# Optimization experiments

Hardware: AMD Instinct MI355X
Metric: run time of the kernel (lower is better)

Reference implementation:

```python
import jax, jax.numpy as jnp
import numpy as np

SEQ_LEN = 256
VOCAB = 50000
EMBED = 300
PROJ = 200
ATT = 200
CLS = 3
B = 128


def setup_inputs() -> dict:
    key = jax.random.key(0)
    ks = jax.random.split(key, 16)
    s = lambda d: 1.0 / np.sqrt(d)
    return {
        "x1": jax.random.randint(ks[0], (B, SEQ_LEN), 0, VOCAB, dtype=jnp.int32),
        "x2": jax.random.randint(ks[1], (B, SEQ_LEN), 0, VOCAB, dtype=jnp.int32),
        "emb": jax.random.normal(ks[2], (VOCAB, EMBED), jnp.float32),
        # intra-attention forward_product FC (shared for x1/x2 via AUTO_REUSE)
        "Wi": jax.random.normal(ks[3], (EMBED, ATT), jnp.float32) * s(EMBED),
        "bi": jnp.zeros((ATT,), jnp.float32),
        "b_dist": jax.random.normal(ks[4], (1,), jnp.float32) * 0.1,
        # embed-scope projection (input is concat[x, xp] -> 2*EMBED), linear
        "Wp": jax.random.normal(ks[5], (2 * EMBED, PROJ), jnp.float32) * s(2 * EMBED),
        "bp": jnp.zeros((PROJ,), jnp.float32),
        # attent forward_product FC (shared)
        "Wa": jax.random.normal(ks[6], (PROJ, ATT), jnp.float32) * s(PROJ),
        "ba": jnp.zeros((ATT,), jnp.float32),
        # compare FC (shared, dim = input dim = 2*PROJ)
        "Wc": jax.random.normal(ks[7], (2 * PROJ, 2 * PROJ), jnp.float32) * s(2 * PROJ),
        "bc": jnp.zeros((2 * PROJ,), jnp.float32),
        # aggregate FC -> class logits (linear)
        "Wg": jax.random.normal(ks[8], (4 * PROJ, CLS), jnp.float32) * s(4 * PROJ),
        "bg": jnp.zeros((CLS,), jnp.float32),
    }


def _seq_mask(x):
    # tf.count_nonzero + tf.sequence_mask -> [B, L, 1] float mask
    size = jnp.sum((x != 0).astype(jnp.float32), axis=1)  # [B]
    m = (jnp.arange(SEQ_LEN)[None, :] < size[:, None]).astype(jnp.float32)
    return m[:, :, None]


def _intra(x, Wi, bi, b_dist):
    # forward_product on (x, x): relu FC then bilinear product -> [B, L, L]
    f = jax.nn.relu(x @ Wi + bi)
    att = jnp.einsum("bid,bjd->bij", f, f)
    idx = jnp.arange(SEQ_LEN)
    dist = jnp.abs(idx[None, :] - idx[:, None])
    bias = b_dist[0] * (dist >= 10).astype(jnp.float32)  # [L, L]
    xp = jnp.einsum("bik,bkj->bij", jax.nn.softmax(att + bias[None], axis=2), x)
    return jnp.concatenate([x, xp], axis=2)  # [B, L, 2*EMBED]


def reference(x1, x2, emb, Wi, bi, b_dist, Wp, bp, Wa, ba, Wc, bc, Wg, bg):
    mask1, mask2 = _seq_mask(x1), _seq_mask(x2)  # [B, L, 1]

    # embedding lookup with L2-normalized table
    emb_n = emb / jnp.linalg.norm(emb, axis=1, keepdims=True)
    e1, e2 = emb_n[x1], emb_n[x2]  # [B, L, EMBED]

    # intra-attention (distance-biased self alignment), doubles feature dim
    h1 = _intra(e1, Wi, bi, b_dist)
    h2 = _intra(e2, Wi, bi, b_dist)

    # linear projection to PROJ
    p1 = h1 @ Wp + bp  # [B, L, PROJ]
    p2 = h2 @ Wp + bp

    # attent: forward_product sim + mask + dual-axis softmax alignments
    a1 = jax.nn.relu(p1 @ Wa + ba)
    a2 = jax.nn.relu(p2 @ Wa + ba)
    sim = jnp.einsum("bid,bjd->bij", a1, a2)  # [B, L, L]
    sim = sim * (mask1 * jnp.swapaxes(mask2, 1, 2))
    alpha = jnp.einsum("bki,bkj->bij", jax.nn.softmax(sim, axis=1), p1)
    beta = jnp.einsum("bik,bkj->bij", jax.nn.softmax(sim, axis=2), p2)

    # compare (shared relu FC)
    v1 = jax.nn.relu(jnp.concatenate([p1, beta], 2) @ Wc + bc)
    v2 = jax.nn.relu(jnp.concatenate([p2, alpha], 2) @ Wc + bc)

    # aggregate: masked sum pooling + linear classifier
    v1 = jnp.sum(v1 * mask1, axis=1)  # [B, 2*PROJ]
    v2 = jnp.sum(v2 * mask2, axis=1)
    return jnp.concatenate([v1, v2], 1) @ Wg + bg  # [B, CLS]
```

## Files before the change

### kernel.cpp

```cpp
#include <hip/hip_runtime.h>
#include <math.h>

#define LSEQ 256
#define NB   128

typedef unsigned short u16;
typedef unsigned int   u32;
typedef __attribute__((ext_vector_type(8))) short bf16x8;
typedef __attribute__((ext_vector_type(4))) float f32x4;

static __device__ __forceinline__ u16 f2bf(float x) {
    union { float f; u32 u; } v; v.f = x;
    const u32 r = v.u + 0x7fffu + ((v.u >> 16) & 1u);
    return (u16)(r >> 16);
}
static __device__ __forceinline__ void glds16(const u16* src, u16* dst) {
    __builtin_amdgcn_global_load_lds(
        (const __attribute__((address_space(1))) u32*)src,
        (__attribute__((address_space(3))) u32*)dst, 16, 0, 0);
}

template<int EPI, bool BIAS, bool RELU>
__global__ __launch_bounds__(512)
void gemm(const u16* __restrict__ A, int lda,
          const u16* __restrict__ B, int ldb,
          u16* __restrict__ C, int ldc,
          const float* __restrict__ bias, int Nbias,
          float* __restrict__ pool, const float* __restrict__ pmask,
          int K, int Nwrite)
{
    __shared__ u16 As[128 * 64];
    __shared__ u16 Bs[256 * 64];

    const int m0 = blockIdx.y * 128;
    const int n0 = blockIdx.x * 256;
    const int t = threadIdx.x;
    const int lane = t & 63;
    const int w = t >> 6;
    const int wm = w >> 2;
    const int wn = w & 3;
    const int lr = lane & 15;
    const int lg = lane >> 4;

    f32x4 acc[4][4] = {};

    for (int k0 = 0; k0 < K; k0 += 64) {
#pragma unroll
        for (int i = 0; i < 2; ++i) {
            const int ch = w * 2 + i;
            const int row = (ch << 3) + (lane >> 3);
            const int slot = (lane & 7) ^ (row & 7);
            glds16(A + (long long)(m0 + row) * lda + k0 + (slot << 3), &As[ch << 9]);
        }
#pragma unroll
        for (int i = 0; i < 4; ++i) {
            const int ch = w * 4 + i;
            const int row = (ch << 3) + (lane >> 3);
            const int slot = (lane & 7) ^ (row & 7);
            glds16(B + (long long)(n0 + row) * ldb + k0 + (slot << 3), &Bs[ch << 9]);
        }
        __syncthreads();
#pragma unroll
        for (int kk = 0; kk < 2; ++kk) {
            bf16x8 af[4], bf[4];
#pragma unroll
            for (int mi = 0; mi < 4; ++mi) {
                const int row = wm * 64 + mi * 16 + lr;
                const int slot = ((kk << 2) + lg) ^ (row & 7);
                af[mi] = *reinterpret_cast<const bf16x8*>(&As[row * 64 + (slot << 3)]);
            }
#pragma unroll
            for (int ni = 0; ni < 4; ++ni) {
                const int row = wn * 64 + ni * 16 + lr;
                const int slot = ((kk << 2) + lg) ^ (row & 7);
                bf[ni] = *reinterpret_cast<const bf16x8*>(&Bs[row * 64 + (slot << 3)]);
            }
#pragma unroll
            for (int mi = 0; mi < 4; ++mi)
#pragma unroll
                for (int ni = 0; ni < 4; ++ni)
                    acc[mi][ni] = __builtin_amdgcn_mfma_f32_16x16x32_bf16(
                        af[mi], bf[ni], acc[mi][ni], 0, 0, 0);
        }
        __syncthreads();
    }

    const int rbase = lg << 2;
    if (EPI == 0) {
#pragma unroll
        for (int ni = 0; ni < 4; ++ni) {
            const int gc = n0 + wn * 64 + ni * 16 + lr;
            if (gc >= Nwrite) continue;
            float bcv = 0.f;
            if (BIAS) bcv = (gc < Nbias) ? bias[gc] : 0.f;
#pragma unroll
            for (int mi = 0; mi < 4; ++mi) {
#pragma unroll
                for (int r = 0; r < 4; ++r) {
                    const long long gr = m0 + wm * 64 + mi * 16 + rbase + r;
                    float x = acc[mi][ni][r];
                    if (BIAS) x += bcv;
                    if (RELU) x = fmaxf(x, 0.f);
                    C[gr * ldc + gc] = f2bf(x);
                }
            }
        }
    } else {
        __syncthreads();
        float* pool_s = reinterpret_cast<float*>(As);
        for (int i = t; i < 256; i += 512) pool_s[i] = 0.f;
        __syncthreads();
        const int b_lin = m0 >> 8;
        const int side  = b_lin >> 7;
        const int bb    = b_lin & 127;
        const float* mk = pmask + b_lin * 256 + (m0 & 255);
        float mrow[4][4];
#pragma unroll
        for (int mi = 0; mi < 4; ++mi)
#pragma unroll
            for (int r = 0; r < 4; ++r)
                mrow[mi][r] = mk[wm * 64 + mi * 16 + rbase + r];
#pragma unroll
        for (int ni = 0; ni < 4; ++ni) {
            const int lc = wn * 64 + ni * 16 + lr;
            const int gc = n0 + lc;
            const float bcv = (BIAS && gc < Nbias) ? bias[gc] : 0.f;
            float cs = 0.f;
#pragma unroll
            for (int mi = 0; mi < 4; ++mi)
#pragma unroll
                for (int r = 0; r < 4; ++r)
                    cs += fmaxf(acc[mi][ni][r] + bcv, 0.f) * mrow[mi][r];
            cs += __shfl_xor(cs, 16, 64);
            cs += __shfl_xor(cs, 32, 64);
            if (lg == 0) atomicAdd(&pool_s[lc], cs);
        }
        __syncthreads();
        for (int i = t; i < 256; i += 512) {
            const int gc = n0 + i;
            if (gc < Nwrite) atomicAdd(&pool[bb * 800 + side * 400 + gc], pool_s[i]);
        }
    }
}

template<int MODE>
__global__ __launch_bounds__(512)
void fattn(const u16* __restrict__ QK, u16* __restrict__ Hb,
           u16* __restrict__ CMP, u16* __restrict__ CMP2,
           const float* __restrict__ M1, const float* __restrict__ M2,
           const float* __restrict__ b_dist)
{
    constexpr int NVT = (MODE == 0) ? 5 : 4;
    __shared__ char shmem[57344];
    u16* Ks = (u16*)shmem;
    u16* Qs = (u16*)(shmem + 32768);
    float* red  = (float*)(shmem + 49152);
    float* red2 = (float*)(shmem + 51200);
    u16* Pc = (u16*)shmem;
    u16* Vc = (u16*)(shmem + 16384);

    const int bz = blockIdx.x;
    int b, half, rowoff, ldv, ldc, Nwrite;
    const u16 *Kp, *Qp, *Vp;
    u16* Cp;
    const float *mrow = nullptr, *mcol = nullptr;
    if (MODE == 0) {
        b = (bz & 7) + (bz >> 4) * 8;
        half = (bz >> 3) & 1;
        Kp = QK + (long long)b * 65536;
        Qp = Kp;
        Vp = Hb + (long long)b * 163840; ldv = 640;
        Cp = Hb + (long long)b * 163840 + half * 128 * 640 + 320;
        ldc = 640; Nwrite = 320; rowoff = half * 128;
    } else {
        const int xcd = bz & 7, j = bz >> 3;
        const int sib = j & 3;
        b = xcd + (j >> 2) * 8;
        half = sib & 1;
        const int v = sib >> 1;
        const u16* a1 = QK + (long long)b * 65536;
        const u16* a2 = QK + 32768LL * 256 + (long long)b * 65536;
        u16* P1 = CMP  + (long long)b * 114688;
        u16* P2 = CMP2 + (long long)b * 114688;
        if (v == 0) { Qp = a1 + half * 128 * 256; Kp = a2; Vp = P2;
                      Cp = P1 + half * 128 * 448 + 200;
                      mrow = M1 + b * 256 + half * 128; mcol = M2 + b * 256; }
        else        { Qp = a2 + half * 128 * 256; Kp = a1; Vp = P1;
                      Cp = P2 + half * 128 * 448 + 200;
                      mrow = M2 + b * 256 + half * 128; mcol = M1 + b * 256; }
        ldv = 448; ldc = 448; Nwrite = 248; rowoff = 0;
    }

    const int t = threadIdx.x, lane = t & 63, w = t >> 6;
    const int lr = lane & 15, lg = lane >> 4;
    const int wk = w >> 1, wr = w & 1;
    const int wr2 = w >> 2, wc = w & 3;

    f32x4 acc[4][4] = {};
    for (int k0 = 0; k0 < 256; k0 += 64) {
#pragma unroll
        for (int i = 0; i < 4; ++i) {
            const int ch = w * 4 + i;
            const int row = (ch << 3) + (lane >> 3);
            const int slot = (lane & 7) ^ (row & 7);
            glds16(Kp + (long long)row * 256 + k0 + (slot << 3), &Ks[ch << 9]);
        }
        if (MODE != 0) {
#pragma unroll
            for (int i = 0; i < 2; ++i) {
                const int ch = w * 2 + i;
                const int row = (ch << 3) + (lane >> 3);
                const int slot = (lane & 7) ^ (row & 7);
                glds16(Qp + (long long)row * 256 + k0 + (slot << 3), &Qs[ch << 9]);
            }
        }
        __syncthreads();
#pragma unroll
        for (int kk = 0; kk < 2; ++kk) {
            bf16x8 kf[4], qf[4];
#pragma unroll
            for (int ki = 0; ki < 4; ++ki) {
                const int row = wk * 64 + ki * 16 + lr;
                const int slot = ((kk << 2) + lg) ^ (row & 7);
                kf[ki] = *reinterpret_cast<const bf16x8*>(&Ks[row * 64 + (slot << 3)]);
            }
#pragma unroll
            for (int qi = 0; qi < 4; ++qi) {
                if (MODE == 0) {
                    const int row = rowoff + wr * 64 + qi * 16 + lr;
                    const int slot = ((kk << 2) + lg) ^ (row & 7);
                    qf[qi] = *reinterpret_cast<const bf16x8*>(&Ks[row * 64 + (slot << 3)]);
                } else {
                    const int row = wr * 64 + qi * 16 + lr;
                    const int slot = ((kk << 2) + lg) ^ (row & 7);
                    qf[qi] = *reinterpret_cast<const bf16x8*>(&Qs[row * 64 + (slot << 3)]);
                }
            }
#pragma unroll
            for (int ki = 0; ki < 4; ++ki)
#pragma unroll
                for (int qi = 0; qi < 4; ++qi)
                    acc[ki][qi] = __builtin_amdgcn_mfma_f32_16x16x32_bf16(
                        kf[ki], qf[qi], acc[ki][qi], 0, 0, 0);
        }
        __syncthreads();
    }

    if (MODE == 1) {
        float mr[4], mc[4][4];
#pragma unroll
        for (int qi = 0; qi < 4; ++qi) mr[qi] = mrow[wr * 64 + qi * 16 + lr];
#pragma unroll
        for (int ki = 0; ki < 4; ++ki)
#pragma unroll
            for (int r = 0; r < 4; ++r)
                mc[ki][r] = mcol[wk * 64 + ki * 16 + (lg << 2) + r];
#pragma unroll
        for (int ki = 0; ki < 4; ++ki)
#pragma unroll
            for (int qi = 0; qi < 4; ++qi)
#pragma unroll
                for (int r = 0; r < 4; ++r)
                    acc[ki][qi][r] *= mr[qi] * mc[ki][r];
    } else {
        const float bd = b_dist[0];
#pragma unroll
        for (int ki = 0; ki < 4; ++ki)
#pragma unroll
            for (int qi = 0; qi < 4; ++qi)
#pragma unroll
                for (int r = 0; r < 4; ++r) {
                    const int irow = rowoff + wr * 64 + qi * 16 + lr;
                    const int jcol = wk * 64 + ki * 16 + (lg << 2) + r;
                    const int d = irow > jcol ? irow - jcol : jcol - irow;
                    if (d >= 10) acc[ki][qi][r] += bd;
                }
    }

    float mx[4];
#pragma unroll
    for (int qi = 0; qi < 4; ++qi) {
        float m_ = -1e30f;
#pragma unroll
        for (int ki = 0; ki < 4; ++ki)
#pragma unroll
            for (int r = 0; r < 4; ++r) m_ = fmaxf(m_, acc[ki][qi][r]);
        m_ = fmaxf(m_, __shfl_xor(m_, 16, 64));
        m_ = fmaxf(m_, __shfl_xor(m_, 32, 64));
        mx[qi] = m_;
    }
    if (lg == 0) {
#pragma unroll
        for (int qi = 0; qi < 4; ++qi)
            red[(wr * 64 + qi * 16 + lr) * 4 + wk] = mx[qi];
    }
    __syncthreads();
    float sm[4];
#pragma unroll
    for (int qi = 0; qi < 4; ++qi) {
        const int row = wr * 64 + qi * 16 + lr;
        const float m_ = fmaxf(fmaxf(red[row * 4 + 0], red[row * 4 + 1]),
                               fmaxf(red[row * 4 + 2], red[row * 4 + 3]));
        float s_ = 0.f;
#pragma unroll
        for (int ki = 0; ki < 4; ++ki)
#pragma unroll
            for (int r = 0; r < 4; ++r) {
                const float e_ = expf(acc[ki][qi][r] - m_);
                acc[ki][qi][r] = e_;
                s_ += e_;
            }
        s_ += __shfl_xor(s_, 16, 64);
        s_ += __shfl_xor(s_, 32, 64);
        sm[qi] = s_;
    }
    if (lg == 0) {
#pragma unroll
        for (int qi = 0; qi < 4; ++qi)
            red2[(wr * 64 + qi * 16 + lr) * 4 + wk] = sm[qi];
    }
    __syncthreads();
#pragma unroll
    for (int qi = 0; qi < 4; ++qi) {
        const int row = wr * 64 + qi * 16 + lr;
        const float rs = 1.0f / (red2[row * 4 + 0] + red2[row * 4 + 1]
                               + red2[row * 4 + 2] + red2[row * 4 + 3]);
#pragma unroll
        for (int ki = 0; ki < 4; ++ki)
#pragma unroll
            for (int r = 0; r < 4; ++r) acc[ki][qi][r] *= rs;
    }
    __syncthreads();

    f32x4 opv[4][NVT] = {};
    for (int c = 0; c < 4; ++c) {
        {
            const int n4 = (t & 63) << 2;
            const int k8 = (t >> 6) << 3;
            union { uint2 q2[8]; u16 s[32]; } uq;
#pragma unroll
            for (int i = 0; i < 8; ++i)
                uq.q2[i] = *reinterpret_cast<const uint2*>(
                    Vp + (long long)(c * 64 + k8 + i) * ldv + n4);
#pragma unroll
            for (int j = 0; j < 4; ++j) {
                const int row = n4 + j;
                const u32 v0 = (u32)uq.s[j]      | ((u32)uq.s[4 + j]  << 16);
                const u32 v1 = (u32)uq.s[8 + j]  | ((u32)uq.s[12 + j] << 16);
                const u32 v2 = (u32)uq.s[16 + j] | ((u32)uq.s[20 + j] << 16);
                const u32 v3 = (u32)uq.s[24 + j] | ((u32)uq.s[28 + j] << 16);
                const int slot = (t >> 6) ^ (row & 7);
                *reinterpret_cast<uint4*>(&Vc[row * 64 + (slot << 3)]) =
                    make_uint4(v0, v1, v2, v3);
            }
            if (NVT == 5 && t < 128) {
                const int n4b = 256 + ((t & 15) << 2);
                const int k8b = (t >> 4) << 3;
                union { uint2 q2[8]; u16 s[32]; } ub;
#pragma unroll
                for (int i = 0; i < 8; ++i)
                    ub.q2[i] = *reinterpret_cast<const uint2*>(
                        Vp + (long long)(c * 64 + k8b + i) * ldv + n4b);
#pragma unroll
                for (int j = 0; j < 4; ++j) {
                    const int row = n4b + j;
                    const u32 v0 = (u32)ub.s[j]      | ((u32)ub.s[4 + j]  << 16);
                    const u32 v1 = (u32)ub.s[8 + j]  | ((u32)ub.s[12 + j] << 16);
                    const u32 v2 = (u32)ub.s[16 + j] | ((u32)ub.s[20 + j] << 16);
                    const u32 v3 = (u32)ub.s[24 + j] | ((u32)ub.s[28 + j] << 16);
                    const int slot = (t >> 4) ^ (row & 7);
                    *reinterpret_cast<uint4*>(&Vc[row * 64 + (slot << 3)]) =
                        make_uint4(v0, v1, v2, v3);
                }
            }
        }
        if (wk == c) {
#pragma unroll
            for (int qi = 0; qi < 4; ++qi) {
                const int qrow = wr * 64 + qi * 16 + lr;
#pragma unroll
                for (int ki = 0; ki < 4; ++ki) {
                    const u32 lo = (u32)f2bf(acc[ki][qi][0]) | ((u32)f2bf(acc[ki][qi][1]) << 16);
                    const u32 hi = (u32)f2bf(acc[ki][qi][2]) | ((u32)f2bf(acc[ki][qi][3]) << 16);
                    const int slot = ((ki << 1) + (lg >> 1)) ^ (qrow & 7);
                    *reinterpret_cast<uint2*>(
                        (char*)Pc + qrow * 128 + (slot << 4) + ((lg & 1) << 3)) =
                        make_uint2(lo, hi);
                }
            }
        }
        __syncthreads();
#pragma unroll
        for (int kk = 0; kk < 2; ++kk) {
            bf16x8 pa[4], vb[NVT];
#pragma unroll
            for (int qi = 0; qi < 4; ++qi) {
                const int row = wr2 * 64 + qi * 16 + lr;
                const int slot = ((kk << 2) + lg) ^ (row & 7);
                pa[qi] = *reinterpret_cast<const bf16x8*>(&Pc[row * 64 + (slot << 3)]);
            }
#pragma unroll
            for (int vi = 0; vi < NVT; ++vi) {
                const int row = wc * (NVT * 16) + vi * 16 + lr;
                const int slot = ((kk << 2) + lg) ^ (row & 7);
                vb[vi] = *reinterpret_cast<const bf16x8*>(&Vc[row * 64 + (slot << 3)]);
            }
#pragma unroll
            for (int qi = 0; qi < 4; ++qi)
#pragma unroll
                for (int vi = 0; vi < NVT; ++vi)
                    opv[qi][vi] = __builtin_amdgcn_mfma_f32_16x16x32_bf16(
                        pa[qi], vb[vi], opv[qi][vi], 0, 0, 0);
        }
        __syncthreads();
    }

#pragma unroll
    for (int qi = 0; qi < 4; ++qi)
#pragma unroll
        for (int vi = 0; vi < NVT; ++vi) {
            const int gc = wc * (NVT * 16) + vi * 16 + lr;
            if (gc >= Nwrite) continue;
#pragma unroll
            for (int r = 0; r < 4; ++r) {
                const int qrow = wr2 * 64 + qi * 16 + (lg << 2) + r;
                Cp[(long long)qrow * ldc + gc] = f2bf(opv[qi][vi][r]);
            }
        }
}

__global__ __launch_bounds__(256)
void prep_w(const float* __restrict__ src, int srcRows, int srcCols,
            u16* __restrict__ dst, int dstCols, int dstTotal,
            int seg1, int seg2start)
{
    const int idx = blockIdx.x * 256 + threadIdx.x;
    if (idx >= dstTotal) return;
    const int n = idx / dstCols, k = idx - n * dstCols;
    int sr = -1;
    if (k < seg1) sr = k;
    else if (k >= seg2start && (k - seg2start) < (srcRows - seg1)) sr = seg1 + (k - seg2start);
    u16 v = 0;
    if (n < srcCols && sr >= 0) v = f2bf(src[(long long)sr * srcCols + n]);
    dst[idx] = v;
}

__global__ __launch_bounds__(256)
void zero_pool(float* __restrict__ p)
{
    p[blockIdx.x * 256 + threadIdx.x] = 0.f;
}

__global__ __launch_bounds__(256)
void make_mask(const int* __restrict__ x, float* __restrict__ mask)
{
    const int b = blockIdx.x;
    const int t = threadIdx.x;
    int nz = (x[b * LSEQ + t] != 0) ? 1 : 0;
#pragma unroll
    for (int o = 32; o; o >>= 1) nz += __shfl_xor(nz, o, 64);
    __shared__ int red[4];
    if ((t & 63) == 0) red[t >> 6] = nz;
    __syncthreads();
    const int size = red[0] + red[1] + red[2] + red[3];
    mask[b * LSEQ + t] = (t < size) ? 1.0f : 0.0f;
}

__global__ __launch_bounds__(256)
void gather_norm(const int* __restrict__ x, const float* __restrict__ emb,
                 u16* __restrict__ h)
{
    const int t = threadIdx.x;
    const int lane = t & 63;
    const long long row = (long long)blockIdx.x * 4 + (t >> 6);
    const int tok = x[row];
    const float* er = emb + (long long)tok * 300;
    float vals[5];
    float ss = 0.f;
#pragma unroll
    for (int i = 0; i < 5; ++i) {
        const int c = lane + i * 64;
        const float v = (c < 300) ? er[c] : 0.f;
        vals[i] = v;
        ss = fmaf(v, v, ss);
    }
#pragma unroll
    for (int o = 32; o; o >>= 1) ss += __shfl_xor(ss, o, 64);
    const float inv = 1.0f / sqrtf(ss);
    u16* out = h + row * 640;
#pragma unroll
    for (int i = 0; i < 5; ++i) {
        const int c = lane + i * 64;
        out[c] = f2bf(vals[i] * inv);
    }
}

__global__ __launch_bounds__(256)
void final_fc(const float* __restrict__ pooled, const float* __restrict__ Wg,
              const float* __restrict__ bg, float* __restrict__ out)
{
    const int b = blockIdx.x;
    const int t = threadIdx.x;
    float a0 = 0.f, a1 = 0.f, a2 = 0.f;
    for (int k = t; k < 800; k += 256) {
        const float p = pooled[(long long)b * 800 + k];
        a0 = fmaf(p, Wg[k * 3 + 0], a0);
        a1 = fmaf(p, Wg[k * 3 + 1], a1);
        a2 = fmaf(p, Wg[k * 3 + 2], a2);
    }
#pragma unroll
    for (int o = 32; o; o >>= 1) {
        a0 += __shfl_xor(a0, o, 64);
        a1 += __shfl_xor(a1, o, 64);
        a2 += __shfl_xor(a2, o, 64);
    }
    __shared__ float r0[4], r1[4], r2[4];
    if ((t & 63) == 0) { r0[t >> 6] = a0; r1[t >> 6] = a1; r2[t >> 6] = a2; }
    __syncthreads();
    if (t == 0) {
        out[b * 3 + 0] = r0[0] + r0[1] + r0[2] + r0[3] + bg[0];
        out[b * 3 + 1] = r1[0] + r1[1] + r1[2] + r1[3] + bg[1];
        out[b * 3 + 2] = r2[0] + r2[1] + r2[2] + r2[3] + bg[2];
    }
}

extern "C" void kernel_launch(void* const* d_in, const int* in_sizes, int n_in,
                              void* d_out, int out_size, void* d_ws, size_t ws_size,
                              hipStream_t stream)
{
    (void)in_sizes; (void)n_in; (void)out_size; (void)ws_size;

    const int*   x1     = (const int*)  d_in[0];
    const int*   x2     = (const int*)  d_in[1];
    const float* emb    = (const float*)d_in[2];
    const float* Wi     = (const float*)d_in[3];
    const float* bi     = (const float*)d_in[4];
    const float* b_dist = (const float*)d_in[5];
    const float* Wp     = (const float*)d_in[6];
    const float* bp     = (const float*)d_in[7];
    const float* Wa     = (const float*)d_in[8];
    const float* ba     = (const float*)d_in[9];
    const float* Wc     = (const float*)d_in[10];
    const float* bc     = (const float*)d_in[11];
    const float* Wg     = (const float*)d_in[12];
    const float* bg     = (const float*)d_in[13];
    float* out = (float*)d_out;

    u16* wsu  = (u16*)d_ws;
    u16* H    = wsu;
    u16* CMP  = wsu + 41943040;
    u16* FA   = wsu + 71303168;
    u16* WiT  = wsu + 88080384;
    u16* WaT  = wsu + 88162304;
    u16* WpT  = wsu + 88227840;
    u16* WcT  = wsu + 88391680;
    float* fb = (float*)(wsu + 88621056);
    float* POOL = fb;
    float* M1f  = fb + 102400;
    float* M2f  = fb + 135168;

    u16* H2   = H   + (long long)32768 * 640;
    u16* CMP2 = CMP + (long long)32768 * 448;

    zero_pool<<<400, 256, 0, stream>>>(POOL);
    make_mask<<<NB, 256, 0, stream>>>(x1, M1f);
    make_mask<<<NB, 256, 0, stream>>>(x2, M2f);
    prep_w<<<(256 * 320) / 256, 256, 0, stream>>>(Wi, 300, 200, WiT, 320, 256 * 320, 300, 320);
    prep_w<<<(256 * 256) / 256, 256, 0, stream>>>(Wa, 200, 200, WaT, 256, 256 * 256, 200, 256);
    prep_w<<<(256 * 640) / 256, 256, 0, stream>>>(Wp, 600, 200, WpT, 640, 256 * 640, 300, 320);
    prep_w<<<(512 * 448) / 256, 256, 0, stream>>>(Wc, 400, 400, WcT, 448, 512 * 448, 400, 448);

    gather_norm<<<8192, 256, 0, stream>>>(x1, emb, H);
    gather_norm<<<8192, 256, 0, stream>>>(x2, emb, H2);

    gemm<0, true, true><<<dim3(1, 512, 1), 512, 0, stream>>>(
        H, 640, WiT, 320, FA, 256, bi, 200, nullptr, nullptr, 320, 256);
    fattn<0><<<512, 512, 0, stream>>>(FA, H, nullptr, nullptr, nullptr, nullptr, b_dist);
    gemm<0, true, false><<<dim3(1, 512, 1), 512, 0, stream>>>(
        H, 640, WpT, 640, CMP, 448, bp, 200, nullptr, nullptr, 640, 256);
    gemm<0, true, true><<<dim3(1, 512, 1), 512, 0, stream>>>(
        CMP, 448, WaT, 256, FA, 256, ba, 200, nullptr, nullptr, 256, 256);
    fattn<1><<<512, 512, 0, stream>>>(FA, nullptr, CMP, CMP2, M1f, M2f, nullptr);
    gemm<2, true, true><<<dim3(2, 512, 1), 512, 0, stream>>>(
        CMP, 448, WcT, 448, nullptr, 0, bc, 400, POOL, M1f, 448, 400);

    final_fc<<<NB, 256, 0, stream>>>(POOL, Wg, bg, out);
}
```

Measured before the change: 237.6 us.

## Prefetch V tiles into registers, use fast exp, and merge prep kernels

The attention kernel now loads the next 64-row V chunk into registers before the barrier, overlapping global loads with softmax and MFMA work. expf is replaced by the fast __expf intrinsic. Mask creation, pool zeroing, the four weight conversions and the two embedding gathers are merged into three launches to cut launch overhead. The changes add register pressure and slightly lower exp precision.

```diff
diff --git a/kernel.cpp b/kernel.cpp
--- a/kernel.cpp
+++ b/kernel.cpp
@@ -277,6 +277,22 @@
                 }
     }
 
+    const int n4  = (t & 63) << 2;
+    const int k8v = (t >> 6) << 3;
+    const int n4b = 256 + ((t & 15) << 2);
+    const int k8b = (t >> 4) << 3;
+    uint2 vreg[8], vtail[8];
+#pragma unroll
+    for (int i = 0; i < 8; ++i)
+        vreg[i] = *reinterpret_cast<const uint2*>(Vp + (long long)(k8v + i) * ldv + n4);
+    if (NVT == 5) {
+        if (t < 128) {
+#pragma unroll
+            for (int i = 0; i < 8; ++i)
+                vtail[i] = *reinterpret_cast<const uint2*>(Vp + (long long)(k8b + i) * ldv + n4b);
+        }
+    }
+
     float mx[4];
 #pragma unroll
     for (int qi = 0; qi < 4; ++qi) {
@@ -306,7 +322,7 @@
         for (int ki = 0; ki < 4; ++ki)
 #pragma unroll
             for (int r = 0; r < 4; ++r) {
-                const float e_ = expf(acc[ki][qi][r] - m_);
+                const float e_ = __expf(acc[ki][qi][r] - m_);
                 acc[ki][qi][r] = e_;
                 s_ += e_;
             }
@@ -335,13 +351,9 @@
     f32x4 opv[4][NVT] = {};
     for (int c = 0; c < 4; ++c) {
         {
-            const int n4 = (t & 63) << 2;
-            const int k8 = (t >> 6) << 3;
             union { uint2 q2[8]; u16 s[32]; } uq;
 #pragma unroll
-            for (int i = 0; i < 8; ++i)
-                uq.q2[i] = *reinterpret_cast<const uint2*>(
-                    Vp + (long long)(c * 64 + k8 + i) * ldv + n4);
+            for (int i = 0; i < 8; ++i) uq.q2[i] = vreg[i];
 #pragma unroll
             for (int j = 0; j < 4; ++j) {
                 const int row = n4 + j;
@@ -354,13 +366,9 @@
                     make_uint4(v0, v1, v2, v3);
             }
             if (NVT == 5 && t < 128) {
-                const int n4b = 256 + ((t & 15) << 2);
-                const int k8b = (t >> 4) << 3;
                 union { uint2 q2[8]; u16 s[32]; } ub;
 #pragma unroll
-                for (int i = 0; i < 8; ++i)
-                    ub.q2[i] = *reinterpret_cast<const uint2*>(
-                        Vp + (long long)(c * 64 + k8b + i) * ldv + n4b);
+                for (int i = 0; i < 8; ++i) ub.q2[i] = vtail[i];
 #pragma unroll
                 for (int j = 0; j < 4; ++j) {
                     const int row = n4b + j;
@@ -389,6 +397,18 @@
                 }
             }
         }
+        if (c < 3) {
+#pragma unroll
+            for (int i = 0; i < 8; ++i)
+                vreg[i] = *reinterpret_cast<const uint2*>(
+                    Vp + (long long)((c + 1) * 64 + k8v + i) * ldv + n4);
+            if (NVT == 5 && t < 128) {
+#pragma unroll
+                for (int i = 0; i < 8; ++i)
+                    vtail[i] = *reinterpret_cast<const uint2*>(
+                        Vp + (long long)((c + 1) * 64 + k8b + i) * ldv + n4b);
+            }
+        }
         __syncthreads();
 #pragma unroll
         for (int kk = 0; kk < 2; ++kk) {
@@ -430,32 +450,14 @@
 }
 
 __global__ __launch_bounds__(256)
-void prep_w(const float* __restrict__ src, int srcRows, int srcCols,
-            u16* __restrict__ dst, int dstCols, int dstTotal,
-            int seg1, int seg2start)
+void prep_small(const int* __restrict__ x1, const int* __restrict__ x2,
+                float* __restrict__ M1f, float* __restrict__ POOL)
 {
-    const int idx = blockIdx.x * 256 + threadIdx.x;
-    if (idx >= dstTotal) return;
-    const int n = idx / dstCols, k = idx - n * dstCols;
-    int sr = -1;
-    if (k < seg1) sr = k;
-    else if (k >= seg2start && (k - seg2start) < (srcRows - seg1)) sr = seg1 + (k - seg2start);
-    u16 v = 0;
-    if (n < srcCols && sr >= 0) v = f2bf(src[(long long)sr * srcCols + n]);
-    dst[idx] = v;
-}
-
-__global__ __launch_bounds__(256)
-void zero_pool(float* __restrict__ p)
-{
-    p[blockIdx.x * 256 + threadIdx.x] = 0.f;
-}
-
-__global__ __launch_bounds__(256)
-void make_mask(const int* __restrict__ x, float* __restrict__ mask)
-{
-    const int b = blockIdx.x;
+    const int blk = blockIdx.x;
+    const int b = blk & 127;
     const int t = threadIdx.x;
+    const int* x = (blk < 128) ? x1 : x2;
+    float* mask = M1f + (blk < 128 ? 0 : 32768);
     int nz = (x[b * LSEQ + t] != 0) ? 1 : 0;
 #pragma unroll
     for (int o = 32; o; o >>= 1) nz += __shfl_xor(nz, o, 64);
@@ -464,16 +466,40 @@
     __syncthreads();
     const int size = red[0] + red[1] + red[2] + red[3];
     mask[b * LSEQ + t] = (t < size) ? 1.0f : 0.0f;
+    if (blk < 128) {
+        for (int i = t; i < 800; i += 256) POOL[b * 800 + i] = 0.f;
+    }
 }
 
 __global__ __launch_bounds__(256)
-void gather_norm(const int* __restrict__ x, const float* __restrict__ emb,
-                 u16* __restrict__ h)
+void prep_weights(const float* __restrict__ Wi, const float* __restrict__ Wa,
+                  const float* __restrict__ Wp, const float* __restrict__ Wc,
+                  u16* __restrict__ WiT, u16* __restrict__ WaT,
+                  u16* __restrict__ WpT, u16* __restrict__ WcT)
+{
+    int idx = blockIdx.x * 256 + threadIdx.x;
+    const float* src; u16* dst; int srcRows, srcCols, dstCols, seg1, seg2;
+    if (idx < 81920)       { src = Wi; dst = WiT; srcRows = 300; srcCols = 200; dstCols = 320; seg1 = 300; seg2 = 320; }
+    else if (idx < 147456) { idx -= 81920;  src = Wa; dst = WaT; srcRows = 200; srcCols = 200; dstCols = 256; seg1 = 200; seg2 = 256; }
+    else if (idx < 311296) { idx -= 147456; src = Wp; dst = WpT; srcRows = 600; srcCols = 200; dstCols = 640; seg1 = 300; seg2 = 320; }
+    else                   { idx -= 311296; src = Wc; dst = WcT; srcRows = 400; srcCols = 400; dstCols = 448; seg1 = 400; seg2 = 448; }
+    const int n = idx / dstCols, k = idx - n * dstCols;
+    int sr = -1;
+    if (k < seg1) sr = k;
+    else if (k >= seg2 && (k - seg2) < (srcRows - seg1)) sr = seg1 + (k - seg2);
+    u16 v = 0;
+    if (n < srcCols && sr >= 0) v = f2bf(src[(long long)sr * srcCols + n]);
+    dst[idx] = v;
+}
+
+__global__ __launch_bounds__(256)
+void gather_norm(const int* __restrict__ x1, const int* __restrict__ x2,
+                 const float* __restrict__ emb, u16* __restrict__ h)
 {
     const int t = threadIdx.x;
     const int lane = t & 63;
     const long long row = (long long)blockIdx.x * 4 + (t >> 6);
-    const int tok = x[row];
+    const int tok = (row < 32768) ? x1[row] : x2[row - 32768];
     const float* er = emb + (long long)tok * 300;
     float vals[5];
     float ss = 0.f;
@@ -559,19 +585,11 @@
     float* M1f  = fb + 102400;
     float* M2f  = fb + 135168;
 
-    u16* H2   = H   + (long long)32768 * 640;
     u16* CMP2 = CMP + (long long)32768 * 448;
 
-    zero_pool<<<400, 256, 0, stream>>>(POOL);
-    make_mask<<<NB, 256, 0, stream>>>(x1, M1f);
-    make_mask<<<NB, 256, 0, stream>>>(x2, M2f);
-    prep_w<<<(256 * 320) / 256, 256, 0, stream>>>(Wi, 300, 200, WiT, 320, 256 * 320, 300, 320);
-    prep_w<<<(256 * 256) / 256, 256, 0, stream>>>(Wa, 200, 200, WaT, 256, 256 * 256, 200, 256);
-    prep_w<<<(256 * 640) / 256, 256, 0, stream>>>(Wp, 600, 200, WpT, 640, 256 * 640, 300, 320);
-    prep_w<<<(512 * 448) / 256, 256, 0, stream>>>(Wc, 400, 400, WcT, 448, 512 * 448, 400, 448);
-
-    gather_norm<<<8192, 256, 0, stream>>>(x1, emb, H);
-    gather_norm<<<8192, 256, 0, stream>>>(x2, emb, H2);
+    prep_small<<<256, 256, 0, stream>>>(x1, x2, M1f, POOL);
+    prep_weights<<<2112, 256, 0, stream>>>(Wi, Wa, Wp, Wc, WiT, WaT, WpT, WcT);
+    gather_norm<<<16384, 256, 0, stream>>>(x1, x2, emb, H);
 
     gemm<0, true, true><<<dim3(1, 512, 1), 512, 0, stream>>>(
         H, 640, WiT, 320, FA, 256, bi, 200, nullptr, nullptr, 320, 256);
```

After: 207.9 us. -12.5%, faster.
